# Performance work log

Hardware: AMD Instinct MI355X
Metric: run time of the kernel (lower is better)

## Reference

```python
import jax, jax.numpy as jnp
import numpy as np
import math

NUM_HEADS = 3
WINDOW = 7


def _shift_masks(ws):
    # row_mask: block mask for windows wrapping across the bottom edge
    half = ws * (ws // 2)  # 21 for ws=7
    row = np.zeros((ws * ws, ws * ws), np.float32)
    row[-half:, :-half] = -np.inf
    row[:-half, -half:] = -np.inf
    # column_mask = rearrange(row, '(r w1) (c w2) -> (w1 r) (w2 c)')
    col = row.reshape(ws, ws, ws, ws).transpose(1, 0, 3, 2).reshape(ws * ws, ws * ws)
    return jnp.asarray(row), jnp.asarray(col)


def setup_inputs() -> dict:
    key = jax.random.key(0)
    ks = jax.random.split(key, 5)
    B, S, E = 64, 3136, 96
    return {
        'x': jax.random.normal(ks[0], (B, S, E), jnp.float32),
        'w1': jax.random.normal(ks[1], (3 * E, E), jnp.float32) * 0.05,
        'b1': jax.random.normal(ks[2], (3 * E,), jnp.float32) * 0.05,
        'w2': jax.random.normal(ks[3], (E, E), jnp.float32) * 0.05,
        'b2': jax.random.normal(ks[4], (E,), jnp.float32) * 0.05,
    }


def reference(x, w1, b1, w2, b2):
    b, S, E = x.shape
    h = w = int(math.sqrt(S))          # 56
    ws = WINDOW
    H = NUM_HEADS
    Eh = E // H                        # head dim = 32
    nh, nw = h // ws, w // ws          # windows per axis = 8
    scale = 1.0 / math.sqrt(E / H)
    # faithful to original: forward shift = -ws//2 = -4, inverse shift = ws//2 = 3
    shift_fwd = -ws // 2
    shift_bwd = ws // 2

    qkv = x @ w1.T + b1                              # [b, S, 3E]
    qkv = qkv.reshape(b, h, w, E, 3)                 # (c K) split, K fastest
    qkv = jnp.roll(qkv, (shift_fwd, shift_fwd), axis=(1, 2))
    # b (nh m1) (nw m2) (H Eh) K -> b H nh nw (m1 m2) Eh K
    qkv = qkv.reshape(b, nh, ws, nw, ws, H, Eh, 3)
    qkv = qkv.transpose(0, 5, 1, 3, 2, 4, 6, 7).reshape(b, H, nh, nw, ws * ws, Eh, 3)
    Q, K, V = qkv[..., 0], qkv[..., 1], qkv[..., 2]

    s = jnp.einsum('bHhwme,bHhwne->bHhwmn', Q, K) * scale  # [b,H,nh,nw,49,49]
    row_mask, col_mask = _shift_masks(ws)
    s = s.at[:, :, -1, :].add(row_mask)   # last row of windows
    s = s.at[:, :, :, -1].add(col_mask)   # last column of windows

    att = jax.nn.softmax(s, axis=-1)
    o = jnp.einsum('bHhwmn,bHhwne->bHhwme', att, V)        # [b,H,nh,nw,49,Eh]
    # b H nh nw (m1 m2) Eh -> b (nh m1) (nw m2) (H Eh)
    o = o.reshape(b, H, nh, nw, ws, ws, Eh)
    o = o.transpose(0, 2, 4, 3, 5, 1, 6).reshape(b, h, w, E)
    o = jnp.roll(o, (shift_bwd, shift_bwd), axis=(1, 2))
    o = o.reshape(b, S, E)
    return o @ w2.T + b2
```

## Files before the change

kernel.cpp:

```cpp
#include <hip/hip_runtime.h>


typedef _Float16 f16;
typedef _Float16 f16x2 __attribute__((ext_vector_type(2)));
typedef _Float16 f16x4 __attribute__((ext_vector_type(4)));
typedef _Float16 f16x8 __attribute__((ext_vector_type(8)));
typedef float f32x4 __attribute__((ext_vector_type(4)));

static __device__ __forceinline__ f32x4 mfma16(f16x8 a, f16x8 b, f32x4 c) {
    return __builtin_amdgcn_mfma_f32_16x16x32_f16(a, b, c, 0, 0, 0);
}
static __device__ __forceinline__ f16x8 cvt8(const float* __restrict__ p) {
    float4 f0 = *(const float4*)(p);
    float4 f1 = *(const float4*)(p + 4);
    f16x8 h;
    h[0]=(f16)f0.x; h[1]=(f16)f0.y; h[2]=(f16)f0.z; h[3]=(f16)f0.w;
    h[4]=(f16)f1.x; h[5]=(f16)f1.y; h[6]=(f16)f1.z; h[7]=(f16)f1.w;
    return h;
}
static __device__ __forceinline__ f16x8 cvt8p(const float4& f0, const float4& f1) {
    f16x8 h;
    h[0]=(f16)f0.x; h[1]=(f16)f0.y; h[2]=(f16)f0.z; h[3]=(f16)f0.w;
    h[4]=(f16)f1.x; h[5]=(f16)f1.y; h[6]=(f16)f1.z; h[7]=(f16)f1.w;
    return h;
}

#define QK_STR 104
#define VT_STR 56
#define SMEM_BYTES 31152
#define OFF_K  10192
#define OFF_VT 20384

union U2 { int i; f16x2 h; };
union U8 { int i[4]; f16x8 h; };

template<bool WS>
__global__ __launch_bounds__(256, 4) void swin_fused(
    const float* __restrict__ x, const float* __restrict__ w1,
    const float* __restrict__ b1, const float* __restrict__ w2,
    const float* __restrict__ b2, float* __restrict__ out,
    const f16* __restrict__ w1p, const f16* __restrict__ w2p,
    const float* __restrict__ b1p)
{
    __shared__ __align__(16) char smem[SMEM_BYTES];
    f16* q_s  = (f16*)(smem);
    f16* k_s  = (f16*)(smem + OFF_K);
    f16* vt_s = (f16*)(smem + OFF_VT);
    f16* o_s  = q_s;

    const int tid  = threadIdx.x;
    const int wv   = tid >> 6;
    const int lane = tid & 63;
    const int lrow = lane & 15;
    const int lq   = lane >> 4;

    const int bx = blockIdx.x;
    const int b  = bx >> 6;
    const int wz = bx & 63;
    const int wh = wz >> 3;
    const int ww = wz & 7;

    const float* xb = x + b * (3136 * 96);

    if (tid < 96) {
        #pragma unroll
        for (int p7 = 49; p7 < 56; ++p7) vt_s[tid * VT_STR + p7] = (f16)0.f;
    }
    if (tid < 8) vt_s[96 * VT_STR + tid] = (f16)0.f;

    {
        f16x8 bf[5][3];
        int   kq[5], cb[5];
        #pragma unroll
        for (int t = 0; t < 5; ++t) {
            int ot = wv + 4 * t;
            if (ot < 18) {
                int kqv = ot / 6;
                kq[t] = kqv;
                cb[t] = (ot - kqv * 6) * 16;
                if constexpr (WS) {
                    #pragma unroll
                    for (int ks = 0; ks < 3; ++ks)
                        bf[t][ks] = *(const f16x8*)(w1p + (ot*16 + lrow)*96 + ks*32 + lq*8);
                } else {
                    int srowA = (ot*16 + lrow - kqv*96) * 3 + kqv;
                    #pragma unroll
                    for (int ks = 0; ks < 3; ++ks)
                        bf[t][ks] = cvt8(w1 + srowA*96 + ks*32 + lq*8);
                }
            } else kq[t] = -1;
        }
        const float* xrow[4];
        #pragma unroll
        for (int pt = 0; pt < 4; ++pt) {
            int p  = pt * 16 + lrow;
            int pc = (p < 49) ? p : 48;
            int i  = pc / 7, j = pc - i * 7;
            int r  = wh * 7 + i + 4; if (r >= 56) r -= 56;
            int c  = ww * 7 + j + 4; if (c >= 56) c -= 56;
            xrow[pt] = xb + (r * 56 + c) * 96;
        }
        float4 xbuf0[3][2], xbuf1[3][2];
        #pragma unroll
        for (int ks = 0; ks < 3; ++ks) {
            xbuf0[ks][0] = *(const float4*)(xrow[0] + ks * 32 + lq * 8);
            xbuf0[ks][1] = *(const float4*)(xrow[0] + ks * 32 + lq * 8 + 4);
        }
        #pragma unroll
        for (int pt = 0; pt < 4; ++pt) {
            float4 (*cur)[2] = (pt & 1) ? xbuf1 : xbuf0;
            float4 (*nxt)[2] = (pt & 1) ? xbuf0 : xbuf1;
            if (pt < 3) {
                #pragma unroll
                for (int ks = 0; ks < 3; ++ks) {
                    nxt[ks][0] = *(const float4*)(xrow[pt+1] + ks * 32 + lq * 8);
                    nxt[ks][1] = *(const float4*)(xrow[pt+1] + ks * 32 + lq * 8 + 4);
                }
            }
            f16x8 xf[3];
            #pragma unroll
            for (int ks = 0; ks < 3; ++ks) xf[ks] = cvt8p(cur[ks][0], cur[ks][1]);
            const int  p   = pt * 16 + lrow;
            const bool pok = (p < 49);
            #pragma unroll
            for (int t = 0; t < 5; ++t) {
                if (kq[t] < 0) continue;
                int ot = wv + 4 * t;
                f32x4 acc = {0.f, 0.f, 0.f, 0.f};
                if (kq[t] == 2) {
                    #pragma unroll
                    for (int ks = 0; ks < 3; ++ks) acc = mfma16(xf[ks], bf[t][ks], acc);
                    float bc;
                    if constexpr (WS) bc = b1p[ot*16 + lrow];
                    else              bc = b1[(ot*16 + lrow - 192)*3 + 2];
                    int cc = cb[t] + lrow;
                    f16x4 pk;
                    #pragma unroll
                    for (int i2 = 0; i2 < 4; ++i2) pk[i2] = (f16)(acc[i2] + bc);
                    int p4 = pt * 16 + lq * 4;
                    if (p4 < 45)       *(f16x4*)(vt_s + cc * VT_STR + p4) = pk;
                    else if (p4 == 48) vt_s[cc * VT_STR + 48] = pk[0];
                } else {
                    #pragma unroll
                    for (int ks = 0; ks < 3; ++ks) acc = mfma16(bf[t][ks], xf[ks], acc);
                    if (pok) {
                        f32x4 br;
                        if constexpr (WS) {
                            br = *(const f32x4*)(b1p + ot*16 + lq*4);
                        } else {
                            #pragma unroll
                            for (int i2 = 0; i2 < 4; ++i2)
                                br[i2] = b1[(ot*16 + lq*4 + i2 - kq[t]*96)*3 + kq[t]];
                        }
                        f16x4 pk;
                        #pragma unroll
                        for (int i2 = 0; i2 < 4; ++i2) pk[i2] = (f16)(acc[i2] + br[i2]);
                        f16* dst = (kq[t] == 0 ? q_s : k_s) + p * QK_STR + cb[t] + lq * 4;
                        *(f16x4*)dst = pk;
                    }
                }
            }
        }
    }
    __syncthreads();

    const bool mrow = (wh == 7), mcol = (ww == 7);
    const float scale = 0.17677669529663687f;
    const int m = wv * 16 + lrow;

    float mv[16];
    {
        const bool am = (m >= 28);
        const bool a4 = (m % 7) >= 4;
        #pragma unroll
        for (int nt = 0; nt < 4; ++nt)
            #pragma unroll
            for (int i2 = 0; i2 < 4; ++i2) {
                int nn = nt * 16 + lq * 4 + i2;
                bool ok = (nn < 49)
                       && (!mrow || (am == (nn >= 28)))
                       && (!mcol || (a4 == ((nn % 7) >= 4)));
                mv[nt*4 + i2] = ok ? 0.f : -3e38f;
            }
    }
    const int idxA = lrow + 32 * (lq & 1);
    const int idxB = idxA + 16;

    f16x8 bq[3];
    #pragma unroll
    for (int hh = 0; hh < 3; ++hh)
        bq[hh] = *(const f16x8*)(q_s + m * QK_STR + hh * 32 + lq * 8);

    f32x4 sc[4];
    #pragma unroll
    for (int nt = 0; nt < 4; ++nt) {
        f16x8 ak = *(const f16x8*)(k_s + (nt*16 + lrow)*QK_STR + lq*8);
        f32x4 z = {0.f, 0.f, 0.f, 0.f};
        sc[nt] = mfma16(ak, bq[0], z);
    }

    #pragma unroll
    for (int hh = 0; hh < 3; ++hh) {
        f16x8 akn[4];
        if (hh < 2) {
            #pragma unroll
            for (int nt = 0; nt < 4; ++nt)
                akn[nt] = *(const f16x8*)(k_s + (nt*16 + lrow)*QK_STR + (hh+1)*32 + lq*8);
        }
        f16x8 va[2][2];
        #pragma unroll
        for (int et = 0; et < 2; ++et) {
            int vrow = hh * 32 + et * 16 + lrow;
            va[et][0] = *(const f16x8*)(vt_s + vrow * VT_STR + lq * 8);
            va[et][1] = *(const f16x8*)(vt_s + vrow * VT_STR + 32 + lq * 8);
        }
        float ev[16];
        #pragma unroll
        for (int nt = 0; nt < 4; ++nt)
            #pragma unroll
            for (int i2 = 0; i2 < 4; ++i2)
                ev[nt*4 + i2] = __expf(fmaf(sc[nt][i2], scale, mv[nt*4 + i2]));
        float ts[8];
        #pragma unroll
        for (int k2 = 0; k2 < 8; ++k2) ts[k2] = ev[2*k2] + ev[2*k2+1];
        #pragma unroll
        for (int k2 = 0; k2 < 4; ++k2) ts[k2] += ts[k2+4];
        float sp = (ts[0] + ts[1]) + (ts[2] + ts[3]);

        int pd[4][2];
        #pragma unroll
        for (int nt = 0; nt < 4; ++nt) {
            U2 u0, u1;
            u0.h[0] = (f16)ev[nt*4+0]; u0.h[1] = (f16)ev[nt*4+1];
            u1.h[0] = (f16)ev[nt*4+2]; u1.h[1] = (f16)ev[nt*4+3];
            pd[nt][0] = u0.i; pd[nt][1] = u1.i;
        }
        U8 ub0, ub1;
        #pragma unroll
        for (int w = 0; w < 4; ++w) {
            int idx = (w < 2) ? idxA : idxB;
            int rr  = w & 1;
            int a0v = __shfl(pd[0][rr], idx);
            int a1v = __shfl(pd[1][rr], idx);
            ub0.i[w] = (lq & 2) ? a1v : a0v;
            int c0v = __shfl(pd[2][rr], idx);
            int c1v = __shfl(pd[3][rr], idx);
            ub1.i[w] = (lq & 2) ? c1v : c0v;
        }
        float ssum = sp;
        ssum += __shfl_xor(ssum, 16);
        ssum += __shfl_xor(ssum, 32);
        float inv = 1.0f / ssum;

        #pragma unroll
        for (int et = 0; et < 2; ++et) {
            f32x4 z = {0.f, 0.f, 0.f, 0.f};
            f32x4 oc = mfma16(va[et][0], ub0.h, z);
            oc = mfma16(va[et][1], ub1.h, oc);
            if (m < 49) {
                f16x4 pk;
                #pragma unroll
                for (int i2 = 0; i2 < 4; ++i2) pk[i2] = (f16)(oc[i2] * inv);
                *(f16x4*)(o_s + m * QK_STR + hh * 32 + et * 16 + lq * 4) = pk;
            }
        }
        if (hh < 2) {
            #pragma unroll
            for (int nt = 0; nt < 4; ++nt) {
                f32x4 z = {0.f, 0.f, 0.f, 0.f};
                sc[nt] = mfma16(akn[nt], bq[hh+1], z);
            }
        }
    }

    {
        f16x8 bo[3];
        #pragma unroll
        for (int ks = 0; ks < 3; ++ks)
            bo[ks] = *(const f16x8*)(o_s + m * QK_STR + ks * 32 + lq * 8);
        int mm2 = (m < 49) ? m : 48;
        int i = mm2 / 7, j = mm2 - i * 7;
        int orow = wh * 7 + i + 3; if (orow >= 56) orow -= 56;
        int ocol = ww * 7 + j + 3; if (ocol >= 56) ocol -= 56;
        float* op = out + (size_t)(b * 3136 + orow * 56 + ocol) * 96;

        f16x8 aw0[3], aw1[3];
        #pragma unroll
        for (int ks = 0; ks < 3; ++ks) {
            if constexpr (WS)
                aw0[ks] = *(const f16x8*)(w2p + lrow*96 + ks*32 + lq*8);
            else
                aw0[ks] = cvt8(w2 + lrow*96 + ks*32 + lq*8);
        }
        #pragma unroll
        for (int ot2 = 0; ot2 < 6; ++ot2) {
            f16x8* cw = (ot2 & 1) ? aw1 : aw0;
            f16x8* nw = (ot2 & 1) ? aw0 : aw1;
            if (ot2 < 5) {
                #pragma unroll
                for (int ks = 0; ks < 3; ++ks) {
                    if constexpr (WS)
                        nw[ks] = *(const f16x8*)(w2p + ((ot2+1)*16 + lrow)*96 + ks*32 + lq*8);
                    else
                        nw[ks] = cvt8(w2 + ((ot2+1)*16 + lrow)*96 + ks*32 + lq*8);
                }
            }
            f32x4 acc = {0.f, 0.f, 0.f, 0.f};
            #pragma unroll
            for (int ks = 0; ks < 3; ++ks) acc = mfma16(cw[ks], bo[ks], acc);
            f32x4 bias = *(const f32x4*)(b2 + ot2 * 16 + lq * 4);
            if (m < 49) {
                f32x4 o4 = acc + bias;
                *(f32x4*)(op + ot2 * 16 + lq * 4) = o4;
            }
        }
    }
}

__global__ void prep_weights(const float* __restrict__ w1, const float* __restrict__ b1,
                             const float* __restrict__ w2,
                             f16* __restrict__ w1p, f16* __restrict__ w2p,
                             float* __restrict__ b1p)
{
    int idx = blockIdx.x * 256 + threadIdx.x;
    if (idx < 27648) {
        int np = idx / 96, k = idx - np * 96;
        int kq = np / 96, c96 = np - kq * 96;
        w1p[idx] = (f16)w1[(c96 * 3 + kq) * 96 + k];
    } else if (idx < 36864) {
        int i2 = idx - 27648;
        w2p[i2] = (f16)w2[i2];
    } else if (idx < 37152) {
        int np = idx - 36864;
        int kq = np / 96, c96 = np - kq * 96;
        b1p[np] = b1[c96 * 3 + kq];
    }
}

extern "C" void kernel_launch(void* const* d_in, const int* in_sizes, int n_in,
                              void* d_out, int out_size, void* d_ws, size_t ws_size,
                              hipStream_t stream) {
    const float* x  = (const float*)d_in[0];
    const float* w1 = (const float*)d_in[1];
    const float* b1 = (const float*)d_in[2];
    const float* w2 = (const float*)d_in[3];
    const float* b2 = (const float*)d_in[4];
    float* out = (float*)d_out;

    const size_t need = 27648u * 2 + 9216u * 2 + 288u * 4;
    if (ws_size >= need) {
        f16*   w1p = (f16*)d_ws;
        f16*   w2p = w1p + 27648;
        float* b1p = (float*)(w2p + 9216);
        prep_weights<<<dim3(146), dim3(256), 0, stream>>>(w1, b1, w2, w1p, w2p, b1p);
        swin_fused<true><<<dim3(4096), dim3(256), 0, stream>>>(
            x, w1, b1, w2, b2, out, w1p, w2p, b1p);
    } else {
        swin_fused<false><<<dim3(4096), dim3(256), 0, stream>>>(
            x, w1, b1, w2, b2, out, nullptr, nullptr, nullptr);
    }
}
```

Baseline: 234.7 us.

## Keep Q and attention output in registers via shuffles, drop Q smem buffer

Each wave now computes its own Q rows directly and hands them to the QK MFMA through cross-lane shuffles, so Q no longer goes through shared memory. The attention output is also passed to the output projection by shuffles rather than an LDS round trip. Shared memory drops from about 31 KB to about 21 KB and launch bounds rise to 6 blocks per CU, aiming for higher occupancy and less LDS traffic. The cost is extra shuffle instructions and more register pressure under a tighter register budget, which could cause spills.

```diff
diff --git a/kernel.cpp b/kernel.cpp
--- a/kernel.cpp
+++ b/kernel.cpp
@@ -27,15 +27,14 @@
 
 #define QK_STR 104
 #define VT_STR 56
-#define SMEM_BYTES 31152
-#define OFF_K  10192
-#define OFF_VT 20384
+#define SMEM_BYTES 20960
+#define OFF_VT 10192
 
 union U2 { int i; f16x2 h; };
 union U8 { int i[4]; f16x8 h; };
 
 template<bool WS>
-__global__ __launch_bounds__(256, 4) void swin_fused(
+__global__ __launch_bounds__(256, 6) void swin_fused(
     const float* __restrict__ x, const float* __restrict__ w1,
     const float* __restrict__ b1, const float* __restrict__ w2,
     const float* __restrict__ b2, float* __restrict__ out,
@@ -43,16 +42,15 @@
     const float* __restrict__ b1p)
 {
     __shared__ __align__(16) char smem[SMEM_BYTES];
-    f16* q_s  = (f16*)(smem);
-    f16* k_s  = (f16*)(smem + OFF_K);
+    f16* k_s  = (f16*)(smem);
     f16* vt_s = (f16*)(smem + OFF_VT);
-    f16* o_s  = q_s;
 
     const int tid  = threadIdx.x;
     const int wv   = tid >> 6;
     const int lane = tid & 63;
     const int lrow = lane & 15;
     const int lq   = lane >> 4;
+    const int m    = wv * 16 + lrow;
 
     const int bx = blockIdx.x;
     const int b  = bx >> 6;
@@ -68,28 +66,24 @@
     }
     if (tid < 8) vt_s[96 * VT_STR + tid] = (f16)0.f;
 
+    const int idxA = lrow + 32 * (lq & 1);
+    const int idxB = idxA + 16;
+
+    f16x8 bq[3];
+
     {
-        f16x8 bf[5][3];
-        int   kq[5], cb[5];
-        #pragma unroll
-        for (int t = 0; t < 5; ++t) {
-            int ot = wv + 4 * t;
-            if (ot < 18) {
-                int kqv = ot / 6;
-                kq[t] = kqv;
-                cb[t] = (ot - kqv * 6) * 16;
-                if constexpr (WS) {
-                    #pragma unroll
-                    for (int ks = 0; ks < 3; ++ks)
-                        bf[t][ks] = *(const f16x8*)(w1p + (ot*16 + lrow)*96 + ks*32 + lq*8);
-                } else {
-                    int srowA = (ot*16 + lrow - kqv*96) * 3 + kqv;
-                    #pragma unroll
-                    for (int ks = 0; ks < 3; ++ks)
-                        bf[t][ks] = cvt8(w1 + srowA*96 + ks*32 + lq*8);
-                }
-            } else kq[t] = -1;
-        }
+        int pcq = (m < 49) ? m : 48;
+        int iq = pcq / 7, jq = pcq - iq * 7;
+        int rq = wh * 7 + iq + 4; if (rq >= 56) rq -= 56;
+        int cq = ww * 7 + jq + 4; if (cq >= 56) cq -= 56;
+        const float* xqr = xb + (rq * 56 + cq) * 96;
+        float4 xq[3][2];
+        #pragma unroll
+        for (int ks = 0; ks < 3; ++ks) {
+            xq[ks][0] = *(const float4*)(xqr + ks * 32 + lq * 8);
+            xq[ks][1] = *(const float4*)(xqr + ks * 32 + lq * 8 + 4);
+        }
+
         const float* xrow[4];
         #pragma unroll
         for (int pt = 0; pt < 4; ++pt) {
@@ -106,6 +100,71 @@
             xbuf0[ks][0] = *(const float4*)(xrow[0] + ks * 32 + lq * 8);
             xbuf0[ks][1] = *(const float4*)(xrow[0] + ks * 32 + lq * 8 + 4);
         }
+
+        f16x8 bf[3][3]; int kqv[3], cb[3], ob[3];
+        #pragma unroll
+        for (int t = 0; t < 3; ++t) {
+            int ot = 6 + wv + 4 * t;
+            int kv = ot / 6;
+            kqv[t] = kv; cb[t] = (ot - kv * 6) * 16; ob[t] = ot * 16;
+            if constexpr (WS) {
+                #pragma unroll
+                for (int ks = 0; ks < 3; ++ks)
+                    bf[t][ks] = *(const f16x8*)(w1p + (ot*16 + lrow)*96 + ks*32 + lq*8);
+            } else {
+                int srowA = (ot*16 + lrow - kv*96) * 3 + kv;
+                #pragma unroll
+                for (int ks = 0; ks < 3; ++ks)
+                    bf[t][ks] = cvt8(w1 + srowA*96 + ks*32 + lq*8);
+            }
+        }
+
+        f16x8 xfq[3];
+        #pragma unroll
+        for (int ks = 0; ks < 3; ++ks) xfq[ks] = cvt8p(xq[ks][0], xq[ks][1]);
+        int qdlo[6], qdhi[6];
+        #pragma unroll
+        for (int ot = 0; ot < 6; ++ot) {
+            f16x8 aq[3];
+            if constexpr (WS) {
+                #pragma unroll
+                for (int ks = 0; ks < 3; ++ks)
+                    aq[ks] = *(const f16x8*)(w1p + (ot*16 + lrow)*96 + ks*32 + lq*8);
+            } else {
+                int srowA = (ot*16 + lrow) * 3;
+                #pragma unroll
+                for (int ks = 0; ks < 3; ++ks)
+                    aq[ks] = cvt8(w1 + srowA*96 + ks*32 + lq*8);
+            }
+            f32x4 acc = {0.f, 0.f, 0.f, 0.f};
+            #pragma unroll
+            for (int ks = 0; ks < 3; ++ks) acc = mfma16(aq[ks], xfq[ks], acc);
+            f32x4 br;
+            if constexpr (WS) {
+                br = *(const f32x4*)(b1p + ot*16 + lq*4);
+            } else {
+                #pragma unroll
+                for (int i2 = 0; i2 < 4; ++i2)
+                    br[i2] = b1[(ot*16 + lq*4 + i2) * 3];
+            }
+            U2 lo, hi;
+            lo.h[0] = (f16)(acc[0] + br[0]); lo.h[1] = (f16)(acc[1] + br[1]);
+            hi.h[0] = (f16)(acc[2] + br[2]); hi.h[1] = (f16)(acc[3] + br[3]);
+            qdlo[ot] = lo.i; qdhi[ot] = hi.i;
+        }
+        #pragma unroll
+        for (int hh = 0; hh < 3; ++hh) {
+            U8 u;
+            #pragma unroll
+            for (int w = 0; w < 4; ++w) {
+                int idx = (w < 2) ? idxA : idxB;
+                int v0 = __shfl((w & 1) ? qdhi[2*hh]     : qdlo[2*hh],     idx);
+                int v1 = __shfl((w & 1) ? qdhi[2*hh + 1] : qdlo[2*hh + 1], idx);
+                u.i[w] = (lq & 2) ? v1 : v0;
+            }
+            bq[hh] = u.h;
+        }
+
         #pragma unroll
         for (int pt = 0; pt < 4; ++pt) {
             float4 (*cur)[2] = (pt & 1) ? xbuf1 : xbuf0;
@@ -123,16 +182,14 @@
             const int  p   = pt * 16 + lrow;
             const bool pok = (p < 49);
             #pragma unroll
-            for (int t = 0; t < 5; ++t) {
-                if (kq[t] < 0) continue;
-                int ot = wv + 4 * t;
+            for (int t = 0; t < 3; ++t) {
                 f32x4 acc = {0.f, 0.f, 0.f, 0.f};
-                if (kq[t] == 2) {
+                if (kqv[t] == 2) {
                     #pragma unroll
                     for (int ks = 0; ks < 3; ++ks) acc = mfma16(xf[ks], bf[t][ks], acc);
                     float bc;
-                    if constexpr (WS) bc = b1p[ot*16 + lrow];
-                    else              bc = b1[(ot*16 + lrow - 192)*3 + 2];
+                    if constexpr (WS) bc = b1p[ob[t] + lrow];
+                    else              bc = b1[(ob[t] + lrow - 192)*3 + 2];
                     int cc = cb[t] + lrow;
                     f16x4 pk;
                     #pragma unroll
@@ -146,17 +203,16 @@
                     if (pok) {
                         f32x4 br;
                         if constexpr (WS) {
-                            br = *(const f32x4*)(b1p + ot*16 + lq*4);
+                            br = *(const f32x4*)(b1p + ob[t] + lq*4);
                         } else {
                             #pragma unroll
                             for (int i2 = 0; i2 < 4; ++i2)
-                                br[i2] = b1[(ot*16 + lq*4 + i2 - kq[t]*96)*3 + kq[t]];
+                                br[i2] = b1[(ob[t] + lq*4 + i2 - 96)*3 + 1];
                         }
                         f16x4 pk;
                         #pragma unroll
                         for (int i2 = 0; i2 < 4; ++i2) pk[i2] = (f16)(acc[i2] + br[i2]);
-                        f16* dst = (kq[t] == 0 ? q_s : k_s) + p * QK_STR + cb[t] + lq * 4;
-                        *(f16x4*)dst = pk;
+                        *(f16x4*)(k_s + p * QK_STR + cb[t] + lq * 4) = pk;
                     }
                 }
             }
@@ -166,7 +222,6 @@
 
     const bool mrow = (wh == 7), mcol = (ww == 7);
     const float scale = 0.17677669529663687f;
-    const int m = wv * 16 + lrow;
 
     float mv[16];
     {
@@ -183,13 +238,8 @@
                 mv[nt*4 + i2] = ok ? 0.f : -3e38f;
             }
     }
-    const int idxA = lrow + 32 * (lq & 1);
-    const int idxB = idxA + 16;
-
-    f16x8 bq[3];
-    #pragma unroll
-    for (int hh = 0; hh < 3; ++hh)
-        bq[hh] = *(const f16x8*)(q_s + m * QK_STR + hh * 32 + lq * 8);
+
+    int odlo[6], odhi[6];
 
     f32x4 sc[4];
     #pragma unroll
@@ -257,12 +307,10 @@
             f32x4 z = {0.f, 0.f, 0.f, 0.f};
             f32x4 oc = mfma16(va[et][0], ub0.h, z);
             oc = mfma16(va[et][1], ub1.h, oc);
-            if (m < 49) {
-                f16x4 pk;
-                #pragma unroll
-                for (int i2 = 0; i2 < 4; ++i2) pk[i2] = (f16)(oc[i2] * inv);
-                *(f16x4*)(o_s + m * QK_STR + hh * 32 + et * 16 + lq * 4) = pk;
-            }
+            U2 lo, hi;
+            lo.h[0] = (f16)(oc[0] * inv); lo.h[1] = (f16)(oc[1] * inv);
+            hi.h[0] = (f16)(oc[2] * inv); hi.h[1] = (f16)(oc[3] * inv);
+            odlo[2*hh + et] = lo.i; odhi[2*hh + et] = hi.i;
         }
         if (hh < 2) {
             #pragma unroll
@@ -276,8 +324,17 @@
     {
         f16x8 bo[3];
         #pragma unroll
-        for (int ks = 0; ks < 3; ++ks)
-            bo[ks] = *(const f16x8*)(o_s + m * QK_STR + ks * 32 + lq * 8);
+        for (int ks = 0; ks < 3; ++ks) {
+            U8 u;
+            #pragma unroll
+            for (int w = 0; w < 4; ++w) {
+                int idx = (w < 2) ? idxA : idxB;
+                int v0 = __shfl((w & 1) ? odhi[2*ks]     : odlo[2*ks],     idx);
+                int v1 = __shfl((w & 1) ? odhi[2*ks + 1] : odlo[2*ks + 1], idx);
+                u.i[w] = (lq & 2) ? v1 : v0;
+            }
+            bo[ks] = u.h;
+        }
         int mm2 = (m < 49) ? m : 48;
         int i = mm2 / 7, j = mm2 - i * 7;
         int orow = wh * 7 + i + 3; if (orow >= 56) orow -= 56;
```

Measured after the change: 346.9 us. 47.8% more time.
